# Kernel tuning notes

Hardware: AMD Instinct MI355X
Metric: run time of the kernel (lower is better)

## Reference

```python
import jax, jax.numpy as jnp
import numpy as np
from jax import lax

EPS = 1e-10
SIGMA_NSQ = 2.0


def _gauss_win(ws, sigma):
    # faithful to fspecial(Filter.GAUSSIAN): integer grid -ws//2+1 .. ws//2
    r = np.arange(-(ws // 2), ws // 2 + 1, dtype=np.float32)
    xx, yy = np.meshgrid(r, r, indexing='ij')
    g = np.exp(-((xx ** 2 + yy ** 2) / (2.0 * sigma ** 2))).astype(np.float32)
    eps = np.finfo(np.float32).eps
    g[g < eps * g.max()] = 0.0
    s = g.sum()
    if s != 0:
        g = g / s
    # filter2 rotates the kernel 180 deg (no-op for this symmetric Gaussian)
    g = np.rot90(g, 2).copy()
    return jnp.asarray(g)[None, None]  # [1,1,ws,ws]


def _conv_valid(img, win):
    return lax.conv_general_dilated(img, win, (1, 1), 'VALID')


def setup_inputs() -> dict:
    key = jax.random.key(0)
    k1, k2, k3 = jax.random.split(key, 3)
    B, C, H, W = 128, 3, 135, 240
    recons = jax.random.uniform(k1, (B, C, H, W), dtype=jnp.float32)
    x = jax.random.uniform(k2, (B, C, H, W), dtype=jnp.float32)
    Wlin = jax.random.normal(k3, (C * H * W, 1), dtype=jnp.float32) * 0.001
    b = jnp.zeros((1,), dtype=jnp.float32)
    return {"recons": recons, "x": x, "W": Wlin, "b": b}


def _vif(recons, x):
    # recons, x: [B, C, H, W]. NOTE: the original code computes downsampled
    # GT/P for scale>1 but never uses them, so every scale operates on the
    # full-resolution images (replicated faithfully here).
    B, C, H, W = recons.shape
    r = recons.reshape(B * C, 1, H, W)
    p = x.reshape(B * C, 1, H, W)
    num = jnp.zeros((B * C,), dtype=recons.dtype)
    den = jnp.zeros((B * C,), dtype=recons.dtype)
    for scale in range(1, 5):
        N = int(2.0 ** (4 - scale + 1) + 1)  # 17, 9, 5, 3
        win = _gauss_win(N, N / 5.0)
        mu1 = _conv_valid(r, win)
        mu2 = _conv_valid(p, win)
        GT_sum_sq = mu1 * mu1
        P_sum_sq = mu2 * mu2
        GT_P_sum_mul = mu1 * mu2
        sigmaGT_sq = _conv_valid(r * r, win) - GT_sum_sq
        sigmaP_sq = _conv_valid(p * p, win) - P_sum_sq
        sigmaGT_P = _conv_valid(r * p, win) - GT_P_sum_mul
        sigmaGT_sq = jnp.maximum(sigmaGT_sq, 0.0)
        sigmaP_sq = jnp.maximum(sigmaP_sq, 0.0)
        g = sigmaGT_P / (sigmaGT_sq + EPS)
        sv_sq = sigmaP_sq - g * sigmaGT_P
        m1 = sigmaGT_sq < EPS
        g = jnp.where(m1, 0.0, g)
        sv_sq = jnp.where(m1, sigmaP_sq, sv_sq)
        sigmaGT_sq = jnp.where(m1, 0.0, sigmaGT_sq)
        m2 = sigmaP_sq < EPS
        g = jnp.where(m2, 0.0, g)
        sv_sq = jnp.where(m2, 0.0, sv_sq)
        m3 = g < 0
        sv_sq = jnp.where(m3, sigmaP_sq, sv_sq)
        g = jnp.where(m3, 0.0, g)
        sv_sq = jnp.where(sv_sq <= EPS, EPS, sv_sq)
        num = num + jnp.sum(jnp.log10(1.0 + g * g * sigmaGT_sq / (sv_sq + SIGMA_NSQ)), axis=(1, 2, 3))
        den = den + jnp.sum(jnp.log10(1.0 + sigmaGT_sq / SIGMA_NSQ), axis=(1, 2, 3))
    vif = (num / den).reshape(B, C)
    return jnp.mean(vif, axis=1)  # per-image VIF (mean over channels)


def reference(recons, x, W, b):
    B = recons.shape[0]
    vif_per_img = _vif(recons, x)            # [B]
    recons_loss = jnp.mean(1.0 - vif_per_img)
    # base_model stand-in: flatten -> linear
    pred_recons = recons.reshape(B, -1) @ W + b
    pred_orig = x.reshape(B, -1) @ W + b
    prediction_loss = jnp.mean((pred_orig - pred_recons) ** 2)
    loss = prediction_loss + recons_loss
    return (loss, recons_loss, prediction_loss)
```

## Files before the change

### kernel.cpp

```cpp
#include <hip/hip_runtime.h>

#define Himg 135
#define Wimg 240
#define Bimg 128
#define Cimg 3
#define BCN (Bimg*Cimg)
#define HW (Himg*Wimg)
#define CHW (Cimg*HW)
#define EPSF 1e-10f

typedef float fvec4 __attribute__((ext_vector_type(4)));
typedef _Float16 hf;
typedef hf h2 __attribute__((ext_vector_type(2)));
typedef hf h4v __attribute__((ext_vector_type(4)));
typedef hf h8 __attribute__((ext_vector_type(8)));
typedef float f4 __attribute__((ext_vector_type(4)));

#define RSTG 77
#define ASTR 72
#define RHP  104
#define APOFF 5760
#define HTOFF 11520
#define SREDO 19840
#define LDSB  39728

__device__ __forceinline__ h2 pkrtz(float a, float b) {
  return __builtin_bit_cast(h2, __builtin_amdgcn_cvt_pkrtz(a, b));
}
__device__ __forceinline__ h4v pkrtz4(float a, float b, float c, float d) {
  h2 lo = pkrtz(a, b), hi = pkrtz(c, d);
  return (h4v){lo[0], lo[1], hi[0], hi[1]};
}

constexpr double cexp(double x) {
  double s = 1.0, t = 1.0;
  for (int i = 1; i < 48; ++i) { t *= x / (double)i; s += t; }
  return s;
}
template<int N>
struct GaussW {
  float inv, rsum;
  constexpr GaussW() : inv(0), rsum(0) {
    const float sig = (float)N / 5.0f;
    inv = 1.0f / (2.0f * sig * sig);
    float ssum = 0.f;
    for (int i = 0; i < N; ++i) {
      float d = (float)(i - N / 2);
      ssum += (float)cexp((double)(-(d * d) * inv));
    }
    rsum = 1.0f / ssum;
  }
};


template<int N>
__device__ __forceinline__ void scale_pass(
    int chunk, int band, const hf* Ar, const hf* Ap, hf* Ht,
    int ln, int quad, int wave, float& numAcc, float& denAcc)
{
  constexpr int OW  = Wimg - N + 1;
  constexpr int OV  = Himg - N + 1;
  constexpr int OV0 = (OV + 1) / 2;
  constexpr GaussW<N> GW{};

  const int OVc  = chunk ? (OV - OV0) : OV0;
  const int TILc = (OVc + 15) / 16;
  const int THTc = TILc + 1;
  const int hoff = chunk ? (OV0 - 58) : 0;
  const f4 zf = {0.f, 0.f, 0.f, 0.f};

  h8 wfrag;
  #pragma unroll
  for (int j = 0; j < 8; ++j) {
    const int di = quad * 8 + j - ln;
    const float fd = (float)(di - N / 2);
    float v = __expf(-(fd * fd) * GW.inv) * GW.rsum;
    v = ((unsigned)di < (unsigned)N) ? v : 0.f;
    wfrag[j] = (hf)v;
  }

  for (int ct = 0; ct < 3; ++ct) {
    __syncthreads();
    for (int t = wave; t < THTc; t += 4) {
      int rowL = hoff + t * 16 + ln;
      if (rowL > RSTG - 1) rowL = RSTG - 1;
      const int ao = rowL * ASTR + ct * 16 + quad * 8;
      h8 ra = *(const h8*)(Ar + ao);
      h8 pa = *(const h8*)(Ap + ao);
      h8 rsq = ra * ra, psq = pa * pa, rp = ra * pa;
      f4 d0 = __builtin_amdgcn_mfma_f32_16x16x32_f16(ra,  wfrag, zf, 0, 0, 0);
      f4 d1 = __builtin_amdgcn_mfma_f32_16x16x32_f16(pa,  wfrag, zf, 0, 0, 0);
      f4 d2 = __builtin_amdgcn_mfma_f32_16x16x32_f16(rsq, wfrag, zf, 0, 0, 0);
      f4 d3 = __builtin_amdgcn_mfma_f32_16x16x32_f16(psq, wfrag, zf, 0, 0, 0);
      f4 d4 = __builtin_amdgcn_mfma_f32_16x16x32_f16(rp,  wfrag, zf, 0, 0, 0);
      hf* hb = Ht + (ln * 5) * RHP + t * 16 + quad * 4;
      *(h4v*)(hb + 0 * RHP) = pkrtz4(d0[0], d0[1], d0[2], d0[3]);
      *(h4v*)(hb + 1 * RHP) = pkrtz4(d1[0], d1[1], d1[2], d1[3]);
      *(h4v*)(hb + 2 * RHP) = pkrtz4(d2[0], d2[1], d2[2], d2[3]);
      *(h4v*)(hb + 3 * RHP) = pkrtz4(d3[0], d3[1], d3[2], d3[3]);
      *(h4v*)(hb + 4 * RHP) = pkrtz4(d4[0], d4[1], d4[2], d4[3]);
    }
    __syncthreads();
    const int ocol = band * 48 + ct * 16 + ln;
    const bool colv = ocol < OW;
    for (int v = wave; v < TILc; v += 4) {
      const int j0 = v * 16;
      f4 C[5];
      #pragma unroll
      for (int c = 0; c < 5; ++c) {
        h8 bf = *(const h8*)(Ht + (ln * 5 + c) * RHP + j0 + quad * 8);
        C[c] = __builtin_amdgcn_mfma_f32_16x16x32_f16(wfrag, bf, zf, 0, 0, 0);
      }
      float numP = 1.f, denP = 1.f;
      #pragma unroll
      for (int reg = 0; reg < 4; ++reg) {
        const int orow = j0 + quad * 4 + reg;
        const bool inb = (orow < OVc) && colv;
        float mu1 = C[0][reg], mu2 = C[1][reg];
        float sGT = fmaxf(C[2][reg] - mu1 * mu1, 0.f);
        float sP  = fmaxf(C[3][reg] - mu2 * mu2, 0.f);
        float sGP = C[4][reg] - mu1 * mu2;
        float A   = sGT + EPSF;
        float t1  = sGP * sGP;
        float D   = A * fmaf(sP + 2.f, A, -t1);
        float numf = 1.f + __fdividef(t1 * sGT, D);
        const bool valid = inb && (fminf(sGT, sP) >= EPSF) && (sGP > 0.f);
        numf = valid ? numf : 1.f;
        float denf = inb ? fmaf(sGT, 0.5f, 1.f) : 1.f;
        numP *= numf;
        denP *= denf;
      }
      numAcc += __log10f(numP);
      denAcc += __log10f(denP);
    }
  }
}

__global__ __launch_bounds__(256, 4) void vif_fat_kernel(
    const float* __restrict__ recons, const float* __restrict__ xim,
    const float* __restrict__ Wl, float* __restrict__ ws)
{
  extern __shared__ hf lds[];
  hf* Ar = lds;
  hf* Ap = lds + APOFF;
  hf* Ht = lds + HTOFF;
  float* sred = (float*)(lds + SREDO);

  const int b     = blockIdx.x;
  const int band  = b % 5;
  const int rest  = b / 5;
  const int chunk = rest & 1;
  const int bc    = rest >> 1;
  const int img   = bc / 3;
  const int tid   = threadIdx.x;
  const int lane  = tid & 63;
  const int ln    = lane & 15;
  const int quad  = lane >> 4;
  const int wave  = tid >> 6;
  const int r0s   = chunk ? 58 : 0;

  const float* rb = recons + bc * HW;
  const float* pb = xim + bc * HW;
  const float* wb = Wl + (bc % 3) * HW;

  float dotAcc = 0.f;
  for (int it = tid; it < RSTG * 8; it += 256) {
    const int row = it >> 3;
    const int c8  = it & 7;
    const int grow = r0s + row;
    int gcol = band * 48 + c8 * 8;
    if (gcol > Wimg - 8) gcol = Wimg - 8;
    const int idx = grow * Wimg + gcol;
    fvec4 r0 = *(const fvec4*)(rb + idx);
    fvec4 r1 = *(const fvec4*)(rb + idx + 4);
    fvec4 p0 = *(const fvec4*)(pb + idx);
    fvec4 p1 = *(const fvec4*)(pb + idx + 4);
    h2 a0 = pkrtz(r0[0], r0[1]), a1 = pkrtz(r0[2], r0[3]);
    h2 a2 = pkrtz(r1[0], r1[1]), a3 = pkrtz(r1[2], r1[3]);
    h2 b0 = pkrtz(p0[0], p0[1]), b1 = pkrtz(p0[2], p0[3]);
    h2 b2 = pkrtz(p1[0], p1[1]), b3 = pkrtz(p1[2], p1[3]);
    *(h8*)(Ar + row * ASTR + c8 * 8) =
        (h8){a0[0], a0[1], a1[0], a1[1], a2[0], a2[1], a3[0], a3[1]};
    *(h8*)(Ap + row * ASTR + c8 * 8) =
        (h8){b0[0], b0[1], b1[0], b1[1], b2[0], b2[1], b3[0], b3[1]};
    const bool rowOwned = chunk ? (grow >= 68) : (grow < 68);
    if (c8 < 6 && rowOwned) {
      fvec4 w0 = *(const fvec4*)(wb + idx);
      fvec4 w1 = *(const fvec4*)(wb + idx + 4);
      dotAcc += (p0[0]-r0[0])*w0[0] + (p0[1]-r0[1])*w0[1]
              + (p0[2]-r0[2])*w0[2] + (p0[3]-r0[3])*w0[3]
              + (p1[0]-r1[0])*w1[0] + (p1[1]-r1[1])*w1[1]
              + (p1[2]-r1[2])*w1[2] + (p1[3]-r1[3])*w1[3];
    }
  }

  float numAcc = 0.f, denAcc = 0.f;
  scale_pass<17>(chunk, band, Ar, Ap, Ht, ln, quad, wave, numAcc, denAcc);
  scale_pass< 9>(chunk, band, Ar, Ap, Ht, ln, quad, wave, numAcc, denAcc);
  scale_pass< 5>(chunk, band, Ar, Ap, Ht, ln, quad, wave, numAcc, denAcc);
  scale_pass< 3>(chunk, band, Ar, Ap, Ht, ln, quad, wave, numAcc, denAcc);

  #pragma unroll
  for (int off = 32; off > 0; off >>= 1) {
    numAcc += __shfl_down(numAcc, off);
    denAcc += __shfl_down(denAcc, off);
    dotAcc += __shfl_down(dotAcc, off);
  }
  __syncthreads();
  if (lane == 0) {
    sred[wave] = numAcc; sred[4 + wave] = denAcc; sred[8 + wave] = dotAcc;
  }
  __syncthreads();
  if (tid == 0) {
    atomicAdd(&ws[bc],        sred[0] + sred[1] + sred[2] + sred[3]);
    atomicAdd(&ws[384 + bc],  sred[4] + sred[5] + sred[6] + sred[7]);
    atomicAdd(&ws[768 + img], sred[8] + sred[9] + sred[10] + sred[11]);
  }
}

__global__ __launch_bounds__(128) void finalize_kernel(
    const float* __restrict__ ws, float* __restrict__ out)
{
  __shared__ float s1[128], s2[128];
  const int t = threadIdx.x;
  float d = ws[768 + t];
  float psq = d * d;
  float vimg = 0.f;
  #pragma unroll
  for (int c = 0; c < 3; ++c) {
    int bc = t * 3 + c;
    vimg += ws[bc] / ws[384 + bc];
  }
  float rl = 1.f - vimg * (1.f / 3.f);
  s1[t] = psq; s2[t] = rl;
  __syncthreads();
  for (int off = 64; off > 0; off >>= 1) {
    if (t < off) { s1[t] += s1[t + off]; s2[t] += s2[t + off]; }
    __syncthreads();
  }
  if (t == 0) {
    float pred = s1[0] * (1.f / 128.f);
    float rec  = s2[0] * (1.f / 128.f);
    out[0] = pred + rec;
    out[1] = rec;
    out[2] = pred;
  }
}

extern "C" void kernel_launch(void* const* d_in, const int* in_sizes, int n_in,
                              void* d_out, int out_size, void* d_ws, size_t ws_size,
                              hipStream_t stream) {
  const float* recons = (const float*)d_in[0];
  const float* x      = (const float*)d_in[1];
  const float* Wl     = (const float*)d_in[2];
  float* ws  = (float*)d_ws;
  float* out = (float*)d_out;

  hipMemsetAsync(d_ws, 0, 896 * sizeof(float), stream);

  vif_fat_kernel<<<BCN * 2 * 5, 256, LDSB, stream>>>(recons, x, Wl, ws);

  finalize_kernel<<<1, 128, 0, stream>>>(ws, out);
}
```

Baseline: 206.8 us.

## Fuse finalize into main kernel via last-block atomic counter and unroll loops

Removes the separate finalize kernel launch. A global atomic ticket now lets the last finishing block do the final reduction, reading partial sums with relaxed atomic loads. The staging and MFMA loops now have compile-time trip counts and are fully unrolled, and part of the per-pixel VIF math uses float2 vectors. The cost is an extra atomic plus fence per block and more code size and register pressure from the unrolling.

```diff
diff --git a/kernel.cpp b/kernel.cpp
--- a/kernel.cpp
+++ b/kernel.cpp
@@ -8,13 +8,15 @@
 #define HW (Himg*Wimg)
 #define CHW (Cimg*HW)
 #define EPSF 1e-10f
+#define TOTB (BCN*2*5)
 
 typedef float fvec4 __attribute__((ext_vector_type(4)));
+typedef float f2 __attribute__((ext_vector_type(2)));
+typedef float f4 __attribute__((ext_vector_type(4)));
 typedef _Float16 hf;
 typedef hf h2 __attribute__((ext_vector_type(2)));
 typedef hf h4v __attribute__((ext_vector_type(4)));
 typedef hf h8 __attribute__((ext_vector_type(8)));
-typedef float f4 __attribute__((ext_vector_type(4)));
 
 #define RSTG 77
 #define ASTR 72
@@ -30,6 +32,9 @@
 __device__ __forceinline__ h4v pkrtz4(float a, float b, float c, float d) {
   h2 lo = pkrtz(a, b), hi = pkrtz(c, d);
   return (h4v){lo[0], lo[1], hi[0], hi[1]};
+}
+__device__ __forceinline__ float aload(const float* p) {
+  return __hip_atomic_load(p, __ATOMIC_RELAXED, __HIP_MEMORY_SCOPE_AGENT);
 }
 
 constexpr double cexp(double x) {
@@ -61,11 +66,13 @@
   constexpr int OW  = Wimg - N + 1;
   constexpr int OV  = Himg - N + 1;
   constexpr int OV0 = (OV + 1) / 2;
+  constexpr int TIL = (OV0 + 15) / 16;
+  constexpr int THT = TIL + 1;
+  constexpr int NHT = (THT + 3) / 4;
+  constexpr int NVT = (TIL + 3) / 4;
   constexpr GaussW<N> GW{};
 
   const int OVc  = chunk ? (OV - OV0) : OV0;
-  const int TILc = (OVc + 15) / 16;
-  const int THTc = TILc + 1;
   const int hoff = chunk ? (OV0 - 58) : 0;
   const f4 zf = {0.f, 0.f, 0.f, 0.f};
 
@@ -81,64 +88,83 @@
 
   for (int ct = 0; ct < 3; ++ct) {
     __syncthreads();
-    for (int t = wave; t < THTc; t += 4) {
-      int rowL = hoff + t * 16 + ln;
-      if (rowL > RSTG - 1) rowL = RSTG - 1;
-      const int ao = rowL * ASTR + ct * 16 + quad * 8;
-      h8 ra = *(const h8*)(Ar + ao);
-      h8 pa = *(const h8*)(Ap + ao);
-      h8 rsq = ra * ra, psq = pa * pa, rp = ra * pa;
-      f4 d0 = __builtin_amdgcn_mfma_f32_16x16x32_f16(ra,  wfrag, zf, 0, 0, 0);
-      f4 d1 = __builtin_amdgcn_mfma_f32_16x16x32_f16(pa,  wfrag, zf, 0, 0, 0);
-      f4 d2 = __builtin_amdgcn_mfma_f32_16x16x32_f16(rsq, wfrag, zf, 0, 0, 0);
-      f4 d3 = __builtin_amdgcn_mfma_f32_16x16x32_f16(psq, wfrag, zf, 0, 0, 0);
-      f4 d4 = __builtin_amdgcn_mfma_f32_16x16x32_f16(rp,  wfrag, zf, 0, 0, 0);
-      hf* hb = Ht + (ln * 5) * RHP + t * 16 + quad * 4;
-      *(h4v*)(hb + 0 * RHP) = pkrtz4(d0[0], d0[1], d0[2], d0[3]);
-      *(h4v*)(hb + 1 * RHP) = pkrtz4(d1[0], d1[1], d1[2], d1[3]);
-      *(h4v*)(hb + 2 * RHP) = pkrtz4(d2[0], d2[1], d2[2], d2[3]);
-      *(h4v*)(hb + 3 * RHP) = pkrtz4(d3[0], d3[1], d3[2], d3[3]);
-      *(h4v*)(hb + 4 * RHP) = pkrtz4(d4[0], d4[1], d4[2], d4[3]);
+    #pragma unroll
+    for (int i = 0; i < NHT; ++i) {
+      const int t = wave + i * 4;
+      if (t < THT) {
+        int rowL = hoff + t * 16 + ln;
+        if (rowL > RSTG - 1) rowL = RSTG - 1;
+        const int ao = rowL * ASTR + ct * 16 + quad * 8;
+        h8 ra = *(const h8*)(Ar + ao);
+        h8 pa = *(const h8*)(Ap + ao);
+        h8 rsq = ra * ra, psq = pa * pa, rp = ra * pa;
+        f4 d0 = __builtin_amdgcn_mfma_f32_16x16x32_f16(ra,  wfrag, zf, 0, 0, 0);
+        f4 d1 = __builtin_amdgcn_mfma_f32_16x16x32_f16(pa,  wfrag, zf, 0, 0, 0);
+        f4 d2 = __builtin_amdgcn_mfma_f32_16x16x32_f16(rsq, wfrag, zf, 0, 0, 0);
+        f4 d3 = __builtin_amdgcn_mfma_f32_16x16x32_f16(psq, wfrag, zf, 0, 0, 0);
+        f4 d4 = __builtin_amdgcn_mfma_f32_16x16x32_f16(rp,  wfrag, zf, 0, 0, 0);
+        hf* hb = Ht + (ln * 5) * RHP + t * 16 + quad * 4;
+        *(h4v*)(hb + 0 * RHP) = pkrtz4(d0[0], d0[1], d0[2], d0[3]);
+        *(h4v*)(hb + 1 * RHP) = pkrtz4(d1[0], d1[1], d1[2], d1[3]);
+        *(h4v*)(hb + 2 * RHP) = pkrtz4(d2[0], d2[1], d2[2], d2[3]);
+        *(h4v*)(hb + 3 * RHP) = pkrtz4(d3[0], d3[1], d3[2], d3[3]);
+        *(h4v*)(hb + 4 * RHP) = pkrtz4(d4[0], d4[1], d4[2], d4[3]);
+      }
     }
     __syncthreads();
     const int ocol = band * 48 + ct * 16 + ln;
     const bool colv = ocol < OW;
-    for (int v = wave; v < TILc; v += 4) {
-      const int j0 = v * 16;
-      f4 C[5];
-      #pragma unroll
-      for (int c = 0; c < 5; ++c) {
-        h8 bf = *(const h8*)(Ht + (ln * 5 + c) * RHP + j0 + quad * 8);
-        C[c] = __builtin_amdgcn_mfma_f32_16x16x32_f16(wfrag, bf, zf, 0, 0, 0);
+    #pragma unroll
+    for (int i = 0; i < NVT; ++i) {
+      const int v = wave + i * 4;
+      if (v < TIL) {
+        const int j0 = v * 16;
+        f4 C[5];
+        #pragma unroll
+        for (int c = 0; c < 5; ++c) {
+          h8 bf = *(const h8*)(Ht + (ln * 5 + c) * RHP + j0 + quad * 8);
+          C[c] = __builtin_amdgcn_mfma_f32_16x16x32_f16(wfrag, bf, zf, 0, 0, 0);
+        }
+        float numP = 1.f, denP = 1.f;
+        const f2 z2 = {0.f, 0.f};
+        #pragma unroll
+        for (int pr2 = 0; pr2 < 2; ++pr2) {
+          f2 mu1 = {C[0][2 * pr2], C[0][2 * pr2 + 1]};
+          f2 mu2 = {C[1][2 * pr2], C[1][2 * pr2 + 1]};
+          f2 m2c = {C[2][2 * pr2], C[2][2 * pr2 + 1]};
+          f2 m3c = {C[3][2 * pr2], C[3][2 * pr2 + 1]};
+          f2 m4c = {C[4][2 * pr2], C[4][2 * pr2 + 1]};
+          f2 sGT = __builtin_elementwise_max(m2c - mu1 * mu1, z2);
+          f2 sP  = __builtin_elementwise_max(m3c - mu2 * mu2, z2);
+          f2 sGP = m4c - mu1 * mu2;
+          f2 A   = sGT + EPSF;
+          f2 t1  = sGP * sGP;
+          f2 D   = A * __builtin_elementwise_fma(sP + 2.f, A, -t1);
+          f2 rn  = t1 * sGT;
+          #pragma unroll
+          for (int e = 0; e < 2; ++e) {
+            const int reg = pr2 * 2 + e;
+            const int orow = j0 + quad * 4 + reg;
+            const bool inb = (orow < OVc) && colv;
+            float numf = 1.f + __fdividef(rn[e], D[e]);
+            const bool valid = inb && (fminf(sGT[e], sP[e]) >= EPSF) && (sGP[e] > 0.f);
+            numf = valid ? numf : 1.f;
+            float denf = inb ? fmaf(sGT[e], 0.5f, 1.f) : 1.f;
+            numP *= numf;
+            denP *= denf;
+          }
+        }
+        numAcc += __log10f(numP);
+        denAcc += __log10f(denP);
       }
-      float numP = 1.f, denP = 1.f;
-      #pragma unroll
-      for (int reg = 0; reg < 4; ++reg) {
-        const int orow = j0 + quad * 4 + reg;
-        const bool inb = (orow < OVc) && colv;
-        float mu1 = C[0][reg], mu2 = C[1][reg];
-        float sGT = fmaxf(C[2][reg] - mu1 * mu1, 0.f);
-        float sP  = fmaxf(C[3][reg] - mu2 * mu2, 0.f);
-        float sGP = C[4][reg] - mu1 * mu2;
-        float A   = sGT + EPSF;
-        float t1  = sGP * sGP;
-        float D   = A * fmaf(sP + 2.f, A, -t1);
-        float numf = 1.f + __fdividef(t1 * sGT, D);
-        const bool valid = inb && (fminf(sGT, sP) >= EPSF) && (sGP > 0.f);
-        numf = valid ? numf : 1.f;
-        float denf = inb ? fmaf(sGT, 0.5f, 1.f) : 1.f;
-        numP *= numf;
-        denP *= denf;
-      }
-      numAcc += __log10f(numP);
-      denAcc += __log10f(denP);
     }
   }
 }
 
 __global__ __launch_bounds__(256, 4) void vif_fat_kernel(
     const float* __restrict__ recons, const float* __restrict__ xim,
-    const float* __restrict__ Wl, float* __restrict__ ws)
+    const float* __restrict__ Wl, float* __restrict__ ws,
+    float* __restrict__ out)
 {
   extern __shared__ hf lds[];
   hf* Ar = lds;
@@ -164,33 +190,37 @@
   const float* wb = Wl + (bc % 3) * HW;
 
   float dotAcc = 0.f;
-  for (int it = tid; it < RSTG * 8; it += 256) {
-    const int row = it >> 3;
-    const int c8  = it & 7;
-    const int grow = r0s + row;
-    int gcol = band * 48 + c8 * 8;
-    if (gcol > Wimg - 8) gcol = Wimg - 8;
-    const int idx = grow * Wimg + gcol;
-    fvec4 r0 = *(const fvec4*)(rb + idx);
-    fvec4 r1 = *(const fvec4*)(rb + idx + 4);
-    fvec4 p0 = *(const fvec4*)(pb + idx);
-    fvec4 p1 = *(const fvec4*)(pb + idx + 4);
-    h2 a0 = pkrtz(r0[0], r0[1]), a1 = pkrtz(r0[2], r0[3]);
-    h2 a2 = pkrtz(r1[0], r1[1]), a3 = pkrtz(r1[2], r1[3]);
-    h2 b0 = pkrtz(p0[0], p0[1]), b1 = pkrtz(p0[2], p0[3]);
-    h2 b2 = pkrtz(p1[0], p1[1]), b3 = pkrtz(p1[2], p1[3]);
-    *(h8*)(Ar + row * ASTR + c8 * 8) =
-        (h8){a0[0], a0[1], a1[0], a1[1], a2[0], a2[1], a3[0], a3[1]};
-    *(h8*)(Ap + row * ASTR + c8 * 8) =
-        (h8){b0[0], b0[1], b1[0], b1[1], b2[0], b2[1], b3[0], b3[1]};
-    const bool rowOwned = chunk ? (grow >= 68) : (grow < 68);
-    if (c8 < 6 && rowOwned) {
-      fvec4 w0 = *(const fvec4*)(wb + idx);
-      fvec4 w1 = *(const fvec4*)(wb + idx + 4);
-      dotAcc += (p0[0]-r0[0])*w0[0] + (p0[1]-r0[1])*w0[1]
-              + (p0[2]-r0[2])*w0[2] + (p0[3]-r0[3])*w0[3]
-              + (p1[0]-r1[0])*w1[0] + (p1[1]-r1[1])*w1[1]
-              + (p1[2]-r1[2])*w1[2] + (p1[3]-r1[3])*w1[3];
+  #pragma unroll
+  for (int i = 0; i < 3; ++i) {
+    const int it = tid + i * 256;
+    if (it < RSTG * 8) {
+      const int row = it >> 3;
+      const int c8  = it & 7;
+      const int grow = r0s + row;
+      int gcol = band * 48 + c8 * 8;
+      if (gcol > Wimg - 8) gcol = Wimg - 8;
+      const int idx = grow * Wimg + gcol;
+      fvec4 r0 = *(const fvec4*)(rb + idx);
+      fvec4 r1 = *(const fvec4*)(rb + idx + 4);
+      fvec4 p0 = *(const fvec4*)(pb + idx);
+      fvec4 p1 = *(const fvec4*)(pb + idx + 4);
+      h2 a0 = pkrtz(r0[0], r0[1]), a1 = pkrtz(r0[2], r0[3]);
+      h2 a2 = pkrtz(r1[0], r1[1]), a3 = pkrtz(r1[2], r1[3]);
+      h2 b0 = pkrtz(p0[0], p0[1]), b1 = pkrtz(p0[2], p0[3]);
+      h2 b2 = pkrtz(p1[0], p1[1]), b3 = pkrtz(p1[2], p1[3]);
+      *(h8*)(Ar + row * ASTR + c8 * 8) =
+          (h8){a0[0], a0[1], a1[0], a1[1], a2[0], a2[1], a3[0], a3[1]};
+      *(h8*)(Ap + row * ASTR + c8 * 8) =
+          (h8){b0[0], b0[1], b1[0], b1[1], b2[0], b2[1], b3[0], b3[1]};
+      const bool rowOwned = chunk ? (grow >= 68) : (grow < 68);
+      if (c8 < 6 && rowOwned) {
+        fvec4 w0 = *(const fvec4*)(wb + idx);
+        fvec4 w1 = *(const fvec4*)(wb + idx + 4);
+        dotAcc += (p0[0]-r0[0])*w0[0] + (p0[1]-r0[1])*w0[1]
+                + (p0[2]-r0[2])*w0[2] + (p0[3]-r0[3])*w0[3]
+                + (p1[0]-r1[0])*w1[0] + (p1[1]-r1[1])*w1[1]
+                + (p1[2]-r1[2])*w1[2] + (p1[3]-r1[3])*w1[3];
+      }
     }
   }
 
@@ -215,30 +245,34 @@
     atomicAdd(&ws[bc],        sred[0] + sred[1] + sred[2] + sred[3]);
     atomicAdd(&ws[384 + bc],  sred[4] + sred[5] + sred[6] + sred[7]);
     atomicAdd(&ws[768 + img], sred[8] + sred[9] + sred[10] + sred[11]);
-  }
-}
-
-__global__ __launch_bounds__(128) void finalize_kernel(
-    const float* __restrict__ ws, float* __restrict__ out)
-{
-  __shared__ float s1[128], s2[128];
-  const int t = threadIdx.x;
-  float d = ws[768 + t];
-  float psq = d * d;
-  float vimg = 0.f;
-  #pragma unroll
-  for (int c = 0; c < 3; ++c) {
-    int bc = t * 3 + c;
-    vimg += ws[bc] / ws[384 + bc];
-  }
-  float rl = 1.f - vimg * (1.f / 3.f);
-  s1[t] = psq; s2[t] = rl;
+    __threadfence();
+    unsigned old = atomicAdd((unsigned*)(ws + 896), 1u);
+    sred[0] = (old == TOTB - 1) ? 1.f : 0.f;
+  }
+  __syncthreads();
+  if (sred[0] == 0.f) return;
+
+  __threadfence();
+  float* s1 = (float*)lds;
+  float* s2 = s1 + 128;
+  if (tid < 128) {
+    float d = aload(ws + 768 + tid);
+    float psq = d * d;
+    float vimg = 0.f;
+    #pragma unroll
+    for (int c = 0; c < 3; ++c) {
+      const int bcx = tid * 3 + c;
+      vimg += aload(ws + bcx) / aload(ws + 384 + bcx);
+    }
+    float rl = 1.f - vimg * (1.f / 3.f);
+    s1[tid] = psq; s2[tid] = rl;
+  }
   __syncthreads();
   for (int off = 64; off > 0; off >>= 1) {
-    if (t < off) { s1[t] += s1[t + off]; s2[t] += s2[t + off]; }
+    if (tid < off) { s1[tid] += s1[tid + off]; s2[tid] += s2[tid + off]; }
     __syncthreads();
   }
-  if (t == 0) {
+  if (tid == 0) {
     float pred = s1[0] * (1.f / 128.f);
     float rec  = s2[0] * (1.f / 128.f);
     out[0] = pred + rec;
@@ -256,9 +290,7 @@
   float* ws  = (float*)d_ws;
   float* out = (float*)d_out;
 
-  hipMemsetAsync(d_ws, 0, 896 * sizeof(float), stream);
-
-  vif_fat_kernel<<<BCN * 2 * 5, 256, LDSB, stream>>>(recons, x, Wl, ws);
-
-  finalize_kernel<<<1, 128, 0, stream>>>(ws, out);
-}
+  hipMemsetAsync(d_ws, 0, 904 * sizeof(float), stream);
+
+  vif_fat_kernel<<<TOTB, 256, LDSB, stream>>>(recons, x, Wl, ws, out);
+}
```

After: 292.5 us. +41.5%, slower.
